# Optimization experiments

Hardware: AMD Instinct MI355X
Metric: run time of the kernel (lower is better)

The kernel has to match this reference:

```python
import jax, jax.numpy as jnp
import numpy as np

N = 5_000_000   # total nodes
B = 16384       # number of graphs
F_X = 4
F_U = 1


def setup_inputs() -> dict:
    key = jax.random.key(0)
    k = jax.random.split(key, 6)
    x = jax.random.normal(k[0], (N, F_X), dtype=jnp.float32)
    batch = jnp.sort(jax.random.randint(k[1], (N,), 0, B)).astype(jnp.int64)
    u = jax.random.normal(k[2], (B, F_U), dtype=jnp.float32)
    d = F_U + F_X  # 5
    W1 = jax.random.normal(k[3], (d, d), dtype=jnp.float32) / np.sqrt(d)
    b1 = jnp.zeros((d,), dtype=jnp.float32)
    W2 = jax.random.normal(k[4], (d, F_U), dtype=jnp.float32) / np.sqrt(d)
    b2 = jnp.zeros((F_U,), dtype=jnp.float32)
    return {"x": x, "batch": batch, "u": u, "W1": W1, "b1": b1, "W2": W2, "b2": b2}


def reference(x, batch, u, W1, b1, W2, b2):
    # scatter_mean(x, batch, dim=0): segment sum / segment count (empty -> 0)
    seg_sum = jax.ops.segment_sum(x, batch, num_segments=B)            # [B, F_x]
    cnt = jax.ops.segment_sum(jnp.ones((x.shape[0],), x.dtype), batch,
                              num_segments=B)                          # [B]
    mean = jnp.where(cnt[:, None] > 0, seg_sum / jnp.maximum(cnt, 1.0)[:, None], 0.0)
    h = jnp.concatenate([u, mean], axis=1)                             # [B, 5]
    h = jax.nn.leaky_relu(h @ W1 + b1, negative_slope=0.1)
    return h @ W2 + b2                                                 # [B, 1]
```

## Files before the change

### kernel.cpp

```cpp
#include <hip/hip_runtime.h>

#define WAVE 64

__global__ void find_starts_kernel(const int* __restrict__ batch,
                                   int* __restrict__ seg_start,
                                   int N, int B) {
    int i = blockIdx.x * blockDim.x + threadIdx.x;
    if (i > N) return;
    int b_prev = (i == 0) ? -1 : batch[i - 1];
    int b_cur  = (i == N) ? B  : batch[i];
    for (int s = b_prev + 1; s <= b_cur; ++s) seg_start[s] = i;
}

__global__ void __launch_bounds__(256)
seg_mean_mlp_kernel(const float4* __restrict__ x,
                    const int* __restrict__ seg_start,
                    const float* __restrict__ u,
                    const float* __restrict__ W1,
                    const float* __restrict__ b1,
                    const float* __restrict__ W2,
                    const float* __restrict__ b2,
                    float* __restrict__ out, int B) {
    const int wid  = (blockIdx.x * blockDim.x + threadIdx.x) / WAVE;
    const int lane = threadIdx.x & (WAVE - 1);
    if (wid >= B) return;

    const int start = seg_start[wid];
    const int end   = seg_start[wid + 1];

    float4 acc = make_float4(0.f, 0.f, 0.f, 0.f);
    for (int i = start + lane; i < end; i += WAVE) {
        float4 v = x[i];
        acc.x += v.x; acc.y += v.y; acc.z += v.z; acc.w += v.w;
    }

    #pragma unroll
    for (int off = 32; off > 0; off >>= 1) {
        acc.x += __shfl_down(acc.x, off);
        acc.y += __shfl_down(acc.y, off);
        acc.z += __shfl_down(acc.z, off);
        acc.w += __shfl_down(acc.w, off);
    }

    if (lane == 0) {
        const int cnt = end - start;
        const float inv = (cnt > 0) ? (1.0f / (float)cnt) : 0.0f;

        float h[5];
        h[0] = u[wid];
        h[1] = acc.x * inv;
        h[2] = acc.y * inv;
        h[3] = acc.z * inv;
        h[4] = acc.w * inv;

        float o = b2[0];
        #pragma unroll
        for (int j = 0; j < 5; ++j) {
            float t = b1[j];
            #pragma unroll
            for (int i = 0; i < 5; ++i) t += h[i] * W1[i * 5 + j];
            t = (t > 0.0f) ? t : 0.1f * t;
            o += t * W2[j];
        }
        out[wid] = o;
    }
}

extern "C" void kernel_launch(void* const* d_in, const int* in_sizes, int n_in,
                              void* d_out, int out_size, void* d_ws, size_t ws_size,
                              hipStream_t stream) {
    const float* x     = (const float*)d_in[0];
    const int*   batch = (const int*)  d_in[1];
    const float* u     = (const float*)d_in[2];
    const float* W1    = (const float*)d_in[3];
    const float* b1    = (const float*)d_in[4];
    const float* W2    = (const float*)d_in[5];
    const float* b2    = (const float*)d_in[6];
    float* out = (float*)d_out;

    const int N = in_sizes[0] / 4;
    const int B = out_size;

    int* seg_start = (int*)d_ws;

    find_starts_kernel<<<(N + 1 + 255) / 256, 256, 0, stream>>>(batch, seg_start, N, B);

    const int threads = 256;
    const int blocks  = (B * WAVE + threads - 1) / threads;
    seg_mean_mlp_kernel<<<blocks, threads, 0, stream>>>(
        (const float4*)x, seg_start, u, W1, b1, W2, b2, out, B);
}
```

Baseline: 148.0 us.

## Replace segment-start pass with per-block binary search fused into reduction kernel

```diff
diff --git a/kernel.cpp b/kernel.cpp
--- a/kernel.cpp
+++ b/kernel.cpp
@@ -1,32 +1,41 @@
 #include <hip/hip_runtime.h>
 
 #define WAVE 64
-
-__global__ void find_starts_kernel(const int* __restrict__ batch,
-                                   int* __restrict__ seg_start,
-                                   int N, int B) {
-    int i = blockIdx.x * blockDim.x + threadIdx.x;
-    if (i > N) return;
-    int b_prev = (i == 0) ? -1 : batch[i - 1];
-    int b_cur  = (i == N) ? B  : batch[i];
-    for (int s = b_prev + 1; s <= b_cur; ++s) seg_start[s] = i;
-}
+#define SEGS_PER_BLOCK 4
 
 __global__ void __launch_bounds__(256)
-seg_mean_mlp_kernel(const float4* __restrict__ x,
-                    const int* __restrict__ seg_start,
-                    const float* __restrict__ u,
-                    const float* __restrict__ W1,
-                    const float* __restrict__ b1,
-                    const float* __restrict__ W2,
-                    const float* __restrict__ b2,
-                    float* __restrict__ out, int B) {
-    const int wid  = (blockIdx.x * blockDim.x + threadIdx.x) / WAVE;
-    const int lane = threadIdx.x & (WAVE - 1);
+fused_segmean_mlp_kernel(const float4* __restrict__ x,
+                         const int* __restrict__ batch,
+                         const float* __restrict__ u,
+                         const float* __restrict__ W1,
+                         const float* __restrict__ b1,
+                         const float* __restrict__ W2,
+                         const float* __restrict__ b2,
+                         float* __restrict__ out,
+                         int N, int B) {
+    __shared__ int bounds[SEGS_PER_BLOCK + 1];
+
+    const int seg_base = blockIdx.x * SEGS_PER_BLOCK;
+    const int t = threadIdx.x;
+
+    if (t <= SEGS_PER_BLOCK) {
+        const int target = seg_base + t;
+        int lo = 0, hi = N;
+        while (lo < hi) {
+            int mid = (lo + hi) >> 1;
+            if (batch[mid] < target) lo = mid + 1; else hi = mid;
+        }
+        bounds[t] = lo;
+    }
+    __syncthreads();
+
+    const int wv   = t / WAVE;
+    const int lane = t & (WAVE - 1);
+    const int wid  = seg_base + wv;
     if (wid >= B) return;
 
-    const int start = seg_start[wid];
-    const int end   = seg_start[wid + 1];
+    const int start = bounds[wv];
+    const int end   = bounds[wv + 1];
 
     float4 acc = make_float4(0.f, 0.f, 0.f, 0.f);
     for (int i = start + lane; i < end; i += WAVE) {
@@ -56,11 +65,11 @@
         float o = b2[0];
         #pragma unroll
         for (int j = 0; j < 5; ++j) {
-            float t = b1[j];
+            float s = b1[j];
             #pragma unroll
-            for (int i = 0; i < 5; ++i) t += h[i] * W1[i * 5 + j];
-            t = (t > 0.0f) ? t : 0.1f * t;
-            o += t * W2[j];
+            for (int i = 0; i < 5; ++i) s += h[i] * W1[i * 5 + j];
+            s = (s > 0.0f) ? s : 0.1f * s;
+            o += s * W2[j];
         }
         out[wid] = o;
     }
@@ -81,12 +90,7 @@
     const int N = in_sizes[0] / 4;
     const int B = out_size;
 
-    int* seg_start = (int*)d_ws;
-
-    find_starts_kernel<<<(N + 1 + 255) / 256, 256, 0, stream>>>(batch, seg_start, N, B);
-
-    const int threads = 256;
-    const int blocks  = (B * WAVE + threads - 1) / threads;
-    seg_mean_mlp_kernel<<<blocks, threads, 0, stream>>>(
-        (const float4*)x, seg_start, u, W1, b1, W2, b2, out, B);
+    const int blocks = (B + SEGS_PER_BLOCK - 1) / SEGS_PER_BLOCK;
+    fused_segmean_mlp_kernel<<<blocks, 256, 0, stream>>>(
+        (const float4*)x, batch, u, W1, b1, W2, b2, out, N, B);
 }
```

After: 153.6 us. 3.8% more time.
